# Kernel optimization log

Measured on AMD Instinct MI355X. Metric: run time of the kernel, lower is better.

## Reference

```python
import jax, jax.numpy as jnp
import numpy as np

B, N, D = 16, 2048, 256  # batch (pairs*2), num_keypoints, descriptor_dim


def setup_inputs() -> dict:
    key = jax.random.key(0)
    k1, k2, k3, k4 = jax.random.split(key, 4)
    descriptors = jax.random.normal(k1, (B, N, D), dtype=jnp.float32)
    mask = jax.random.randint(k2, (B, N), 0, 2, dtype=jnp.int32)
    proj_w = jax.random.normal(k3, (D, D), dtype=jnp.float32) * 0.02
    proj_b = jnp.zeros((D,), dtype=jnp.float32)
    match_w = jax.random.normal(k4, (1, D), dtype=jnp.float32) * 0.02
    match_b = jnp.zeros((1,), dtype=jnp.float32)
    return {"descriptors": descriptors, "mask": mask, "proj_w": proj_w,
            "proj_b": proj_b, "match_w": match_w, "match_b": match_b}


def reference(descriptors, mask, proj_w, proj_b, match_w, match_b):
    batch, n, d = descriptors.shape
    pairs = batch // 2
    # final projection + temperature scaling
    m_desc = (descriptors @ proj_w.T + proj_b) / jnp.asarray(d, descriptors.dtype) ** 0.25
    m_desc = m_desc.reshape(pairs, 2, n, d)
    # similarity: [pairs, n0, n1]
    similarity = jnp.einsum('bnd,bmd->bnm', m_desc[:, 0], m_desc[:, 1])
    mask_p = mask.reshape(pairs, 2, n)
    pair_mask = mask_p[:, 0][:, :, None] * mask_p[:, 1][:, None, :]
    neg_min = jnp.finfo(similarity.dtype).min
    similarity = jnp.where(pair_mask == 0, neg_min, similarity)
    # matchability logits: [B, n, 1] -> split per pair
    matchability = (descriptors @ match_w.T + match_b).reshape(pairs, 2, n)
    m0 = matchability[:, 0]  # [pairs, n]
    m1 = matchability[:, 1]  # [pairs, n]
    certainties = jax.nn.log_sigmoid(m0)[:, :, None] + jax.nn.log_sigmoid(m1)[:, None, :]
    scores0 = jax.nn.log_softmax(similarity, axis=2)
    scores1 = jax.nn.log_softmax(similarity, axis=1)
    inner = scores0 + scores1 + certainties
    scores = jnp.zeros((pairs, n + 1, n + 1), dtype=similarity.dtype)
    scores = scores.at[:, :n, :n].set(inner)
    scores = scores.at[:, :-1, -1].set(jax.nn.log_sigmoid(-m0))
    scores = scores.at[:, -1, :-1].set(jax.nn.log_sigmoid(-m1))
    return scores
```

## Files before the change

kernel.cpp:

```cpp
#include <hip/hip_runtime.h>
#include <math.h>

typedef unsigned short u16;
typedef __attribute__((ext_vector_type(8))) short bf16x8;
typedef __attribute__((ext_vector_type(4))) float f32x4;

#define BN 16
#define N 2048
#define D 256
#define PAIRS 8
#define NO 2049
#define NEGMIN  -3.40282347e38f
#define MASKVAL -3.0e38f
#define LDA 72

#define WS_LS0   0
#define WS_LS1   (1*PAIRS*N)
#define WS_LSN0  (2*PAIRS*N)
#define WS_LSN1  (3*PAIRS*N)
#define WS_RMAX  (4*PAIRS*N)
#define WS_RLSE  (5*PAIRS*N)
#define WS_CMAX  (6*PAIRS*N)
#define WS_CLSE  (7*PAIRS*N)
#define WS_CPM   (8*PAIRS*N)
#define WS_CPS   (WS_CPM + PAIRS*16*N)
#define WS_F_COUNT (WS_CPS + PAIRS*16*N)

__device__ __forceinline__ float b2f(u16 u) {
    return __uint_as_float(((unsigned)u) << 16);
}
__device__ __forceinline__ u16 f2b(float f) {
    unsigned x = __float_as_uint(f);
    x += 0x7FFFu + ((x >> 16) & 1u);
    return (u16)(x >> 16);
}
__device__ __forceinline__ unsigned pk2(float a, float b) {
    return (unsigned)f2b(a) | ((unsigned)f2b(b) << 16);
}
__device__ __forceinline__ float logsig(float x) {
    return fminf(x, 0.f) - log1pf(expf(-fabsf(x)));
}
__device__ __forceinline__ void online1(float& m, float& s, float x) {
    float nm = fmaxf(m, x);
    float e = __expf(fminf(m, x) - nm);
    s = (x > m) ? s * e + 1.f : s + e;
    m = nm;
}
__device__ __forceinline__ void onmerge(float& m, float& s, float om, float os) {
    float nm = fmaxf(m, om);
    s = s * __expf(m - nm) + os * __expf(om - nm);
    m = nm;
}

__global__ __launch_bounds__(256) void k_match(const float* __restrict__ desc,
                                               const float* __restrict__ mw,
                                               const float* __restrict__ mb,
                                               float* __restrict__ wsf) {
    int row = blockIdx.x * 4 + (threadIdx.x >> 6);
    int lane = threadIdx.x & 63;
    float4 d = *(const float4*)(desc + (size_t)row * D + lane * 4);
    float4 w = *(const float4*)(mw + lane * 4);
    float s = d.x * w.x + d.y * w.y + d.z * w.z + d.w * w.w;
    #pragma unroll
    for (int off = 32; off > 0; off >>= 1) s += __shfl_down(s, off, 64);
    if (lane == 0) {
        float m = s + mb[0];
        int b = row >> 11;
        int i = row & (N - 1);
        int p = b >> 1, sid = b & 1;
        float ls = logsig(m), lsn = logsig(-m);
        if (sid == 0) { wsf[WS_LS0 + p*N + i] = ls; wsf[WS_LSN0 + p*N + i] = lsn; }
        else          { wsf[WS_LS1 + p*N + i] = ls; wsf[WS_LSN1 + p*N + i] = lsn; }
    }
}

__global__ __launch_bounds__(256) void k_proj_mfma(const float* __restrict__ A,
                                                   const float* __restrict__ W,
                                                   const float* __restrict__ bias,
                                                   u16* __restrict__ mdesc) {
    __shared__ u16 As[128 * LDA];
    __shared__ u16 Bs[128 * LDA];
    int r0 = blockIdx.x * 128, c0 = blockIdx.y * 128;
    int tid = threadIdx.x;
    int w = tid >> 6, lane = tid & 63;
    int ln = lane & 15, q = lane >> 4;
    int wr0 = (w >> 1) * 64, wc0 = (w & 1) * 64;
    f32x4 zero = {0.f, 0.f, 0.f, 0.f};
    f32x4 acc[4][4];
    #pragma unroll
    for (int a = 0; a < 4; ++a)
        #pragma unroll
        for (int b = 0; b < 4; ++b) acc[a][b] = zero;

    for (int kb = 0; kb < D; kb += 64) {
        __syncthreads();
        #pragma unroll
        for (int t = 0; t < 4; ++t) {
            int c = t * 256 + tid;
            int row = c >> 3, part = c & 7;
            const float* ap = A + (size_t)(r0 + row) * D + kb + part * 8;
            float4 f0 = *(const float4*)ap;
            float4 f1 = *(const float4*)(ap + 4);
            uint4 va;
            va.x = pk2(f0.x, f0.y); va.y = pk2(f0.z, f0.w);
            va.z = pk2(f1.x, f1.y); va.w = pk2(f1.z, f1.w);
            *(uint4*)&As[row * LDA + part * 8] = va;
            const float* bp = W + (size_t)(c0 + row) * D + kb + part * 8;
            float4 g0 = *(const float4*)bp;
            float4 g1 = *(const float4*)(bp + 4);
            uint4 vb;
            vb.x = pk2(g0.x, g0.y); vb.y = pk2(g0.z, g0.w);
            vb.z = pk2(g1.x, g1.y); vb.w = pk2(g1.z, g1.w);
            *(uint4*)&Bs[row * LDA + part * 8] = vb;
        }
        __syncthreads();
        #pragma unroll
        for (int kk = 0; kk < 64; kk += 32) {
            bf16x8 af[4], bf[4];
            #pragma unroll
            for (int ri = 0; ri < 4; ++ri)
                af[ri] = *(const bf16x8*)&As[(wr0 + ri*16 + ln) * LDA + kk + q*8];
            #pragma unroll
            for (int ci = 0; ci < 4; ++ci)
                bf[ci] = *(const bf16x8*)&Bs[(wc0 + ci*16 + ln) * LDA + kk + q*8];
            #pragma unroll
            for (int ri = 0; ri < 4; ++ri)
                #pragma unroll
                for (int ci = 0; ci < 4; ++ci)
                    acc[ri][ci] = __builtin_amdgcn_mfma_f32_16x16x32_bf16(af[ri], bf[ci], acc[ri][ci], 0, 0, 0);
        }
    }
    #pragma unroll
    for (int ri = 0; ri < 4; ++ri) {
        #pragma unroll
        for (int reg = 0; reg < 4; ++reg) {
            int row = r0 + wr0 + ri*16 + q*4 + reg;
            #pragma unroll
            for (int ci = 0; ci < 4; ++ci) {
                int col = c0 + wc0 + ci*16 + ln;
                float v = (acc[ri][ci][reg] + bias[col]) * 0.25f;
                mdesc[(size_t)row * D + col] = f2b(v);
            }
        }
    }
}

__global__ __launch_bounds__(256) void k_sim_mfma(const u16* __restrict__ mdesc,
                                                  const int* __restrict__ mask,
                                                  u16* __restrict__ out) {
    __shared__ u16 As[128 * LDA];
    __shared__ u16 Bs[128 * LDA];
    int p = blockIdx.z;
    const u16* A  = mdesc + (size_t)(2*p) * N * D;
    const u16* Bm = mdesc + (size_t)(2*p + 1) * N * D;
    int r0 = blockIdx.x * 128, c0 = blockIdx.y * 128;
    int tid = threadIdx.x;
    int w = tid >> 6, lane = tid & 63;
    int ln = lane & 15, q = lane >> 4;
    int wr0 = (w >> 1) * 64, wc0 = (w & 1) * 64;
    f32x4 zero = {0.f, 0.f, 0.f, 0.f};
    f32x4 acc[4][4];
    #pragma unroll
    for (int a = 0; a < 4; ++a)
        #pragma unroll
        for (int b = 0; b < 4; ++b) acc[a][b] = zero;

    for (int kb = 0; kb < D; kb += 64) {
        __syncthreads();
        #pragma unroll
        for (int t = 0; t < 4; ++t) {
            int c = t * 256 + tid;
            int row = c >> 3, part = c & 7;
            uint4 va = *(const uint4*)(A  + (size_t)(r0 + row) * D + kb + part * 8);
            *(uint4*)&As[row * LDA + part * 8] = va;
            uint4 vb = *(const uint4*)(Bm + (size_t)(c0 + row) * D + kb + part * 8);
            *(uint4*)&Bs[row * LDA + part * 8] = vb;
        }
        __syncthreads();
        #pragma unroll
        for (int kk = 0; kk < 64; kk += 32) {
            bf16x8 af[4], bf[4];
            #pragma unroll
            for (int ri = 0; ri < 4; ++ri)
                af[ri] = *(const bf16x8*)&As[(wr0 + ri*16 + ln) * LDA + kk + q*8];
            #pragma unroll
            for (int ci = 0; ci < 4; ++ci)
                bf[ci] = *(const bf16x8*)&Bs[(wc0 + ci*16 + ln) * LDA + kk + q*8];
            #pragma unroll
            for (int ri = 0; ri < 4; ++ri)
                #pragma unroll
                for (int ci = 0; ci < 4; ++ci)
                    acc[ri][ci] = __builtin_amdgcn_mfma_f32_16x16x32_bf16(af[ri], bf[ci], acc[ri][ci], 0, 0, 0);
        }
    }
    const int* m0 = mask + (size_t)(2*p) * N;
    const int* m1 = mask + (size_t)(2*p + 1) * N;
    u16* outp = out + (size_t)p * NO * NO;
    int mcol[4];
    #pragma unroll
    for (int ci = 0; ci < 4; ++ci) mcol[ci] = m1[c0 + wc0 + ci*16 + ln];
    #pragma unroll
    for (int ri = 0; ri < 4; ++ri) {
        #pragma unroll
        for (int reg = 0; reg < 4; ++reg) {
            int row = r0 + wr0 + ri*16 + q*4 + reg;
            int mr = m0[row];
            size_t base = (size_t)row * NO + c0 + wc0 + ln;
            #pragma unroll
            for (int ci = 0; ci < 4; ++ci) {
                float v = (mr && mcol[ci]) ? acc[ri][ci][reg] : MASKVAL;
                outp[base + ci*16] = f2b(v);
            }
        }
    }
}

__global__ __launch_bounds__(256) void k_rowstats(const u16* __restrict__ out,
                                                  float* __restrict__ wsf) {
    int i = blockIdx.x * 4 + (threadIdx.x >> 6);
    int p = blockIdx.y;
    int lane = threadIdx.x & 63;
    size_t B0 = ((size_t)p * NO + i) * NO;
    const unsigned* up = (const unsigned*)out;
    int head = (int)(B0 & 1);
    size_t U0 = (B0 + head) >> 1;
    int nu = (2048 - head) >> 1;
    float m = NEGMIN, s = 0.f;
    for (int k = lane; k < nu; k += 64) {
        unsigned v = up[U0 + k];
        online1(m, s, b2f((u16)v));
        online1(m, s, b2f((u16)(v >> 16)));
    }
    if (head && lane == 0) {
        online1(m, s, b2f(out[B0]));
        online1(m, s, b2f(out[B0 + 2047]));
    }
    #pragma unroll
    for (int off = 32; off > 0; off >>= 1) {
        float om = __shfl_down(m, off, 64);
        float os = __shfl_down(s, off, 64);
        onmerge(m, s, om, os);
    }
    if (lane == 0) {
        wsf[WS_RMAX + p * N + i] = m;
        wsf[WS_RLSE + p * N + i] = logf(s);
    }
}

__global__ __launch_bounds__(256) void k_colstats(const u16* __restrict__ out,
                                                  float* __restrict__ wsf) {
    int cc = blockIdx.x;
    int rc = blockIdx.y;
    int p  = blockIdx.z;
    int c = cc * 256 + threadIdx.x;
    const u16* op = out + (size_t)p * NO * NO + c;
    size_t base = (size_t)rc * 128 * NO;
    float m = NEGMIN, s = 0.f;
    for (int r = 0; r < 128; ++r)
        online1(m, s, b2f(op[base + (size_t)r * NO]));
    wsf[WS_CPM + ((size_t)(p * 16 + rc)) * N + c] = m;
    wsf[WS_CPS + ((size_t)(p * 16 + rc)) * N + c] = s;
}

__global__ __launch_bounds__(256) void k_colred(float* __restrict__ wsf) {
    int cc = blockIdx.x, p = blockIdx.y;
    int c = cc * 256 + threadIdx.x;
    float m = NEGMIN, s = 0.f;
    for (int rc = 0; rc < 16; ++rc)
        onmerge(m, s, wsf[WS_CPM + ((size_t)(p*16 + rc)) * N + c],
                      wsf[WS_CPS + ((size_t)(p*16 + rc)) * N + c]);
    wsf[WS_CMAX + p * N + c] = m;
    wsf[WS_CLSE + p * N + c] = logf(s);
}

__global__ __launch_bounds__(256) void k_final(u16* __restrict__ out,
                                               const float* __restrict__ wsf) {
    int i = blockIdx.x, p = blockIdx.y;
    int tid = threadIdx.x;
    size_t B0 = ((size_t)p * NO + i) * NO;
    unsigned* up = (unsigned*)out;
    int head = (int)(B0 & 1);
    size_t U0 = (B0 + head) >> 1;
    if (i < N) {
        float rm  = wsf[WS_RMAX + p*N + i];
        float rl  = wsf[WS_RLSE + p*N + i];
        float l0  = wsf[WS_LS0  + p*N + i];
        float ln0 = wsf[WS_LSN0 + p*N + i];
        for (int k = tid; k < 1024; k += 256) {
            unsigned v = up[U0 + k];
            int j0 = 2*k + head;
            float o0, o1;
            {
                float x = b2f((u16)v);
                float a = (x - rm) - rl;
                float b = (x - wsf[WS_CMAX + p*N + j0]) - wsf[WS_CLSE + p*N + j0];
                o0 = fmaxf(fmaxf(a + b, MASKVAL) + (l0 + wsf[WS_LS1 + p*N + j0]), MASKVAL);
            }
            int j1 = j0 + 1;
            if (j1 < N) {
                float x = b2f((u16)(v >> 16));
                float a = (x - rm) - rl;
                float b = (x - wsf[WS_CMAX + p*N + j1]) - wsf[WS_CLSE + p*N + j1];
                o1 = fmaxf(fmaxf(a + b, MASKVAL) + (l0 + wsf[WS_LS1 + p*N + j1]), MASKVAL);
            } else {
                o1 = ln0;
            }
            up[U0 + k] = pk2(o0, o1);
        }
        if (tid == 0) {
            if (head) {
                float x = b2f(out[B0]);
                float a = (x - rm) - rl;
                float b = (x - wsf[WS_CMAX + p*N]) - wsf[WS_CLSE + p*N];
                out[B0] = f2b(fmaxf(fmaxf(a + b, MASKVAL) + (l0 + wsf[WS_LS1 + p*N]), MASKVAL));
            } else {
                out[B0 + N] = f2b(ln0);
            }
        }
    } else {
        for (int k = tid; k < 1024; k += 256) {
            int j0 = 2*k + head;
            float o0 = (j0 < N) ? wsf[WS_LSN1 + p*N + j0] : 0.f;
            int j1 = j0 + 1;
            float o1 = (j1 < N) ? wsf[WS_LSN1 + p*N + j1] : 0.f;
            up[U0 + k] = pk2(o0, o1);
        }
        if (tid == 0) {
            if (head) out[B0] = f2b(wsf[WS_LSN1 + p*N]);
            else      out[B0 + N] = 0;
        }
    }
}

extern "C" void kernel_launch(void* const* d_in, const int* in_sizes, int n_in,
                              void* d_out, int out_size, void* d_ws, size_t ws_size,
                              hipStream_t stream) {
    const float* desc    = (const float*)d_in[0];
    const int*   mask    = (const int*)d_in[1];
    const float* proj_w  = (const float*)d_in[2];
    const float* proj_b  = (const float*)d_in[3];
    const float* match_w = (const float*)d_in[4];
    const float* match_b = (const float*)d_in[5];
    u16*   out = (u16*)d_out;
    float* wsf = (float*)d_ws;
    u16*   mdesc = (u16*)((char*)d_ws + (size_t)WS_F_COUNT * sizeof(float));

    k_match    <<<dim3(8192),        256, 0, stream>>>(desc, match_w, match_b, wsf);
    k_proj_mfma<<<dim3(256, 2),      256, 0, stream>>>(desc, proj_w, proj_b, mdesc);
    k_sim_mfma <<<dim3(16, 16, 8),   256, 0, stream>>>(mdesc, mask, out);
    k_rowstats <<<dim3(512, 8),      256, 0, stream>>>(out, wsf);
    k_colstats <<<dim3(8, 16, 8),    256, 0, stream>>>(out, wsf);
    k_colred   <<<dim3(8, 8),        256, 0, stream>>>(wsf);
    k_final    <<<dim3(2049, 8),     256, 0, stream>>>(out, wsf);
}
```

Before: 299.5 us.

## Fuse row/column softmax stats into similarity GEMM epilogue and matchability into projection

Row and column online max/sum-exp partials are now computed from the fp32 accumulators in the similarity GEMM epilogue, using shuffles and shared memory, and written as per-tile partials. A single reduction kernel then merges them. This removes two full passes that re-read the 2049x2049 bf16 score matrix. The matchability dot product is folded into the projection kernel's load loop, which drops a separate pass over the descriptors. In exchange the stats now come from unrounded fp32 values rather than the stored bf16 values, and the GEMM epilogue becomes heavier.

```diff
diff --git a/kernel.cpp b/kernel.cpp
--- a/kernel.cpp
+++ b/kernel.cpp
@@ -22,7 +22,9 @@
 #define WS_RLSE  (5*PAIRS*N)
 #define WS_CMAX  (6*PAIRS*N)
 #define WS_CLSE  (7*PAIRS*N)
-#define WS_CPM   (8*PAIRS*N)
+#define WS_RPM   (8*PAIRS*N)
+#define WS_RPS   (WS_RPM + PAIRS*16*N)
+#define WS_CPM   (WS_RPS + PAIRS*16*N)
 #define WS_CPS   (WS_CPM + PAIRS*16*N)
 #define WS_F_COUNT (WS_CPS + PAIRS*16*N)
 
@@ -52,32 +54,13 @@
     m = nm;
 }
 
-__global__ __launch_bounds__(256) void k_match(const float* __restrict__ desc,
-                                               const float* __restrict__ mw,
-                                               const float* __restrict__ mb,
-                                               float* __restrict__ wsf) {
-    int row = blockIdx.x * 4 + (threadIdx.x >> 6);
-    int lane = threadIdx.x & 63;
-    float4 d = *(const float4*)(desc + (size_t)row * D + lane * 4);
-    float4 w = *(const float4*)(mw + lane * 4);
-    float s = d.x * w.x + d.y * w.y + d.z * w.z + d.w * w.w;
-    #pragma unroll
-    for (int off = 32; off > 0; off >>= 1) s += __shfl_down(s, off, 64);
-    if (lane == 0) {
-        float m = s + mb[0];
-        int b = row >> 11;
-        int i = row & (N - 1);
-        int p = b >> 1, sid = b & 1;
-        float ls = logsig(m), lsn = logsig(-m);
-        if (sid == 0) { wsf[WS_LS0 + p*N + i] = ls; wsf[WS_LSN0 + p*N + i] = lsn; }
-        else          { wsf[WS_LS1 + p*N + i] = ls; wsf[WS_LSN1 + p*N + i] = lsn; }
-    }
-}
-
 __global__ __launch_bounds__(256) void k_proj_mfma(const float* __restrict__ A,
                                                    const float* __restrict__ W,
                                                    const float* __restrict__ bias,
-                                                   u16* __restrict__ mdesc) {
+                                                   const float* __restrict__ mw,
+                                                   const float* __restrict__ mb,
+                                                   u16* __restrict__ mdesc,
+                                                   float* __restrict__ wsf) {
     __shared__ u16 As[128 * LDA];
     __shared__ u16 Bs[128 * LDA];
     int r0 = blockIdx.x * 128, c0 = blockIdx.y * 128;
@@ -91,6 +74,8 @@
     for (int a = 0; a < 4; ++a)
         #pragma unroll
         for (int b = 0; b < 4; ++b) acc[a][b] = zero;
+    float mdot[4] = {0.f, 0.f, 0.f, 0.f};
+    int domatch = (blockIdx.y == 0);
 
     for (int kb = 0; kb < D; kb += 64) {
         __syncthreads();
@@ -105,6 +90,12 @@
             va.x = pk2(f0.x, f0.y); va.y = pk2(f0.z, f0.w);
             va.z = pk2(f1.x, f1.y); va.w = pk2(f1.z, f1.w);
             *(uint4*)&As[row * LDA + part * 8] = va;
+            if (domatch) {
+                float4 w0 = *(const float4*)(mw + kb + part * 8);
+                float4 w1 = *(const float4*)(mw + kb + part * 8 + 4);
+                mdot[t] += f0.x*w0.x + f0.y*w0.y + f0.z*w0.z + f0.w*w0.w
+                         + f1.x*w1.x + f1.y*w1.y + f1.z*w1.z + f1.w*w1.w;
+            }
             const float* bp = W + (size_t)(c0 + row) * D + kb + part * 8;
             float4 g0 = *(const float4*)bp;
             float4 g1 = *(const float4*)(bp + 4);
@@ -130,6 +121,25 @@
                     acc[ri][ci] = __builtin_amdgcn_mfma_f32_16x16x32_bf16(af[ri], bf[ci], acc[ri][ci], 0, 0, 0);
         }
     }
+    if (domatch) {
+        #pragma unroll
+        for (int t = 0; t < 4; ++t) {
+            float s = mdot[t];
+            s += __shfl_xor(s, 1, 64);
+            s += __shfl_xor(s, 2, 64);
+            s += __shfl_xor(s, 4, 64);
+            if ((tid & 7) == 0) {
+                int row_g = r0 + t * 32 + (tid >> 3);
+                float m = s + mb[0];
+                int b = row_g >> 11;
+                int i = row_g & (N - 1);
+                int pp = b >> 1, sid = b & 1;
+                float ls = logsig(m), lsn = logsig(-m);
+                if (sid == 0) { wsf[WS_LS0 + pp*N + i] = ls; wsf[WS_LSN0 + pp*N + i] = lsn; }
+                else          { wsf[WS_LS1 + pp*N + i] = ls; wsf[WS_LSN1 + pp*N + i] = lsn; }
+            }
+        }
+    }
     #pragma unroll
     for (int ri = 0; ri < 4; ++ri) {
         #pragma unroll
@@ -147,9 +157,12 @@
 
 __global__ __launch_bounds__(256) void k_sim_mfma(const u16* __restrict__ mdesc,
                                                   const int* __restrict__ mask,
-                                                  u16* __restrict__ out) {
+                                                  u16* __restrict__ out,
+                                                  float* __restrict__ wsf) {
     __shared__ u16 As[128 * LDA];
     __shared__ u16 Bs[128 * LDA];
+    __shared__ float rpm[128][2], rps[128][2];
+    __shared__ float cpm[128][2], cps[128][2];
     int p = blockIdx.z;
     const u16* A  = mdesc + (size_t)(2*p) * N * D;
     const u16* Bm = mdesc + (size_t)(2*p + 1) * N * D;
@@ -209,68 +222,85 @@
             #pragma unroll
             for (int ci = 0; ci < 4; ++ci) {
                 float v = (mr && mcol[ci]) ? acc[ri][ci][reg] : MASKVAL;
+                acc[ri][ci][reg] = v;
                 outp[base + ci*16] = f2b(v);
             }
         }
     }
-}
-
-__global__ __launch_bounds__(256) void k_rowstats(const u16* __restrict__ out,
-                                                  float* __restrict__ wsf) {
-    int i = blockIdx.x * 4 + (threadIdx.x >> 6);
+    #pragma unroll
+    for (int ri = 0; ri < 4; ++ri) {
+        #pragma unroll
+        for (int reg = 0; reg < 4; ++reg) {
+            float m = acc[ri][0][reg], s = 1.f;
+            online1(m, s, acc[ri][1][reg]);
+            online1(m, s, acc[ri][2][reg]);
+            online1(m, s, acc[ri][3][reg]);
+            #pragma unroll
+            for (int off = 1; off <= 8; off <<= 1) {
+                float om = __shfl_xor(m, off, 64);
+                float os = __shfl_xor(s, off, 64);
+                onmerge(m, s, om, os);
+            }
+            if (ln == 0) {
+                int rl = wr0 + ri*16 + q*4 + reg;
+                rpm[rl][w & 1] = m; rps[rl][w & 1] = s;
+            }
+        }
+    }
+    #pragma unroll
+    for (int ci = 0; ci < 4; ++ci) {
+        float m = acc[0][ci][0], s = 1.f;
+        #pragma unroll
+        for (int ri = 0; ri < 4; ++ri)
+            #pragma unroll
+            for (int reg = 0; reg < 4; ++reg)
+                if (!(ri == 0 && reg == 0)) online1(m, s, acc[ri][ci][reg]);
+        #pragma unroll
+        for (int off = 16; off <= 32; off <<= 1) {
+            float om = __shfl_xor(m, off, 64);
+            float os = __shfl_xor(s, off, 64);
+            onmerge(m, s, om, os);
+        }
+        if (q == 0) {
+            int cl = wc0 + ci*16 + ln;
+            cpm[cl][w >> 1] = m; cps[cl][w >> 1] = s;
+        }
+    }
+    __syncthreads();
+    if (tid < 128) {
+        float m = rpm[tid][0], s = rps[tid][0];
+        onmerge(m, s, rpm[tid][1], rps[tid][1]);
+        size_t o = (size_t)(p * 16 + blockIdx.y) * N + r0 + tid;
+        wsf[WS_RPM + o] = m; wsf[WS_RPS + o] = s;
+    } else {
+        int c = tid - 128;
+        float m = cpm[c][0], s = cps[c][0];
+        onmerge(m, s, cpm[c][1], cps[c][1]);
+        size_t o = (size_t)(p * 16 + blockIdx.x) * N + c0 + c;
+        wsf[WS_CPM + o] = m; wsf[WS_CPS + o] = s;
+    }
+}
+
+__global__ __launch_bounds__(256) void k_red(float* __restrict__ wsf) {
+    int i = blockIdx.x * 256 + threadIdx.x;
     int p = blockIdx.y;
-    int lane = threadIdx.x & 63;
-    size_t B0 = ((size_t)p * NO + i) * NO;
-    const unsigned* up = (const unsigned*)out;
-    int head = (int)(B0 & 1);
-    size_t U0 = (B0 + head) >> 1;
-    int nu = (2048 - head) >> 1;
-    float m = NEGMIN, s = 0.f;
-    for (int k = lane; k < nu; k += 64) {
-        unsigned v = up[U0 + k];
-        online1(m, s, b2f((u16)v));
-        online1(m, s, b2f((u16)(v >> 16)));
-    }
-    if (head && lane == 0) {
-        online1(m, s, b2f(out[B0]));
-        online1(m, s, b2f(out[B0 + 2047]));
-    }
-    #pragma unroll
-    for (int off = 32; off > 0; off >>= 1) {
-        float om = __shfl_down(m, off, 64);
-        float os = __shfl_down(s, off, 64);
-        onmerge(m, s, om, os);
-    }
-    if (lane == 0) {
+    if (blockIdx.z == 0) {
+        float m = wsf[WS_RPM + (size_t)(p*16) * N + i];
+        float s = wsf[WS_RPS + (size_t)(p*16) * N + i];
+        for (int cb = 1; cb < 16; ++cb)
+            onmerge(m, s, wsf[WS_RPM + (size_t)(p*16 + cb) * N + i],
+                          wsf[WS_RPS + (size_t)(p*16 + cb) * N + i]);
         wsf[WS_RMAX + p * N + i] = m;
         wsf[WS_RLSE + p * N + i] = logf(s);
-    }
-}
-
-__global__ __launch_bounds__(256) void k_colstats(const u16* __restrict__ out,
-                                                  float* __restrict__ wsf) {
-    int cc = blockIdx.x;
-    int rc = blockIdx.y;
-    int p  = blockIdx.z;
-    int c = cc * 256 + threadIdx.x;
-    const u16* op = out + (size_t)p * NO * NO + c;
-    size_t base = (size_t)rc * 128 * NO;
-    float m = NEGMIN, s = 0.f;
-    for (int r = 0; r < 128; ++r)
-        online1(m, s, b2f(op[base + (size_t)r * NO]));
-    wsf[WS_CPM + ((size_t)(p * 16 + rc)) * N + c] = m;
-    wsf[WS_CPS + ((size_t)(p * 16 + rc)) * N + c] = s;
-}
-
-__global__ __launch_bounds__(256) void k_colred(float* __restrict__ wsf) {
-    int cc = blockIdx.x, p = blockIdx.y;
-    int c = cc * 256 + threadIdx.x;
-    float m = NEGMIN, s = 0.f;
-    for (int rc = 0; rc < 16; ++rc)
-        onmerge(m, s, wsf[WS_CPM + ((size_t)(p*16 + rc)) * N + c],
-                      wsf[WS_CPS + ((size_t)(p*16 + rc)) * N + c]);
-    wsf[WS_CMAX + p * N + c] = m;
-    wsf[WS_CLSE + p * N + c] = logf(s);
+    } else {
+        float m = wsf[WS_CPM + (size_t)(p*16) * N + i];
+        float s = wsf[WS_CPS + (size_t)(p*16) * N + i];
+        for (int rb = 1; rb < 16; ++rb)
+            onmerge(m, s, wsf[WS_CPM + (size_t)(p*16 + rb) * N + i],
+                          wsf[WS_CPS + (size_t)(p*16 + rb) * N + i]);
+        wsf[WS_CMAX + p * N + i] = m;
+        wsf[WS_CLSE + p * N + i] = logf(s);
+    }
 }
 
 __global__ __launch_bounds__(256) void k_final(u16* __restrict__ out,
@@ -345,11 +375,8 @@
     float* wsf = (float*)d_ws;
     u16*   mdesc = (u16*)((char*)d_ws + (size_t)WS_F_COUNT * sizeof(float));
 
-    k_match    <<<dim3(8192),        256, 0, stream>>>(desc, match_w, match_b, wsf);
-    k_proj_mfma<<<dim3(256, 2),      256, 0, stream>>>(desc, proj_w, proj_b, mdesc);
-    k_sim_mfma <<<dim3(16, 16, 8),   256, 0, stream>>>(mdesc, mask, out);
-    k_rowstats <<<dim3(512, 8),      256, 0, stream>>>(out, wsf);
-    k_colstats <<<dim3(8, 16, 8),    256, 0, stream>>>(out, wsf);
-    k_colred   <<<dim3(8, 8),        256, 0, stream>>>(wsf);
-    k_final    <<<dim3(2049, 8),     256, 0, stream>>>(out, wsf);
-}
+    k_proj_mfma<<<dim3(256, 2),    256, 0, stream>>>(desc, proj_w, proj_b, match_w, match_b, mdesc, wsf);
+    k_sim_mfma <<<dim3(16, 16, 8), 256, 0, stream>>>(mdesc, mask, out, wsf);
+    k_red      <<<dim3(8, 8, 2),   256, 0, stream>>>(wsf);
+    k_final    <<<dim3(2049, 8),   256, 0, stream>>>(out, wsf);
+}
```

Result: faster. 275.3 us (-8.1%).
